# Kernel optimization log

Hardware: AMD Instinct MI355X
Metric: run time of the kernel (lower is better)

## Reference

```python
import jax, jax.numpy as jnp
import numpy as np

EPS = 1e-5  # nn.LayerNorm default
TOP_K = 2


def setup_inputs() -> dict:
    key = jax.random.key(0)
    ks = jax.random.split(key, 8)
    B, S, D, H, E = 4, 2048, 512, 512, 8
    sd = lambda fan_in: 1.0 / np.sqrt(fan_in)
    x = jax.random.normal(ks[0], (B, S, D), dtype=jnp.float32)
    # gate: Linear(D, E, bias=False)
    Wg = jax.random.uniform(ks[1], (D, E), jnp.float32, -sd(D), sd(D))
    # stacked expert params (ExpertModule): fc1 D->H, fc2 H->D, LayerNorm(D)
    W1 = jax.random.uniform(ks[2], (E, D, H), jnp.float32, -sd(D), sd(D))
    b1 = jax.random.uniform(ks[3], (E, H), jnp.float32, -sd(D), sd(D))
    W2 = jax.random.uniform(ks[4], (E, H, D), jnp.float32, -sd(H), sd(H))
    b2 = jax.random.uniform(ks[5], (E, D), jnp.float32, -sd(H), sd(H))
    gamma = jnp.ones((E, D), jnp.float32)
    beta = jnp.zeros((E, D), jnp.float32)
    return {"x": x, "Wg": Wg, "W1": W1, "b1": b1, "W2": W2, "b2": b2,
            "gamma": gamma, "beta": beta}


def _moe_forward(x, Wg, W1, b1, W2, b2, gamma, beta):
    B, S, D = x.shape
    xf = x.reshape(-1, D)                                   # [T, D]
    # gating: top-k logits then softmax over the k selected logits only
    logits = xf @ Wg                                        # [T, E]
    topv, topi = jax.lax.top_k(logits, TOP_K)               # [T, K]
    gate_w = jax.nn.softmax(topv, axis=-1)                  # [T, K]
    # expert MLP + LayerNorm computed for all experts (dropout inactive in eval)
    h = jax.nn.relu(jnp.einsum('td,edh->teh', xf, W1) + b1[None])   # [T, E, H]
    y = jnp.einsum('teh,ehd->ted', h, W2) + b2[None]                 # [T, E, D]
    mu = jnp.mean(y, axis=-1, keepdims=True)
    var = jnp.mean((y - mu) ** 2, axis=-1, keepdims=True)
    y = (y - mu) / jnp.sqrt(var + EPS) * gamma[None] + beta[None]
    # combine: gather the k selected expert outputs and weight-sum
    y_sel = jnp.take_along_axis(y, topi[:, :, None], axis=1)        # [T, K, D]
    out = jnp.sum(gate_w[:, :, None] * y_sel, axis=1)               # [T, D]
    return out.reshape(B, S, D)


def reference(x, Wg, W1, b1, W2, b2, gamma, beta):
    return _moe_forward(x, Wg, W1, b1, W2, b2, gamma, beta)
```

## Files before the change

### kernel.cpp

```cpp
#include <hip/hip_runtime.h>
#include <hip/hip_bf16.h>


#define T_TOK   8192
#define DDIM    512
#define HDIM    512
#define NEXP    8
#define NASSIGN (T_TOK * 2)
#define CPAD    16

typedef _Float16 f16x8 __attribute__((ext_vector_type(8)));
typedef _Float16 f16x4 __attribute__((ext_vector_type(4)));
typedef float    f32x4 __attribute__((ext_vector_type(4)));

__device__ __forceinline__ void gld_lds16(const _Float16* g, _Float16* l) {
    __builtin_amdgcn_global_load_lds(
        (const __attribute__((address_space(1))) unsigned int*)g,
        (__attribute__((address_space(3))) unsigned int*)l,
        16, 0, 0);
}

__global__ __launch_bounds__(256) void prep_kernel(
    const float* __restrict__ x,
    const float* __restrict__ Wg,
    const float* __restrict__ W1,
    const float* __restrict__ W2,
    _Float16* __restrict__ xh,
    int* __restrict__ ei,
    float* __restrict__ gw,
    int* __restrict__ counts,
    _Float16* __restrict__ W1t,
    _Float16* __restrict__ W2t)
{
    __shared__ float wgt[NEXP][512];
    __shared__ float tile[32][33];
    __shared__ int lcnt[NEXP];

    int bid = blockIdx.x;
    int tid = threadIdx.x;

    if (bid < 2048) {
        if (tid < NEXP) lcnt[tid] = 0;
#pragma unroll
        for (int r = 0; r < 2; r++) {
            int d = r * 256 + tid;
            const float4* wr = (const float4*)(Wg + (size_t)d * NEXP);
            float4 a = wr[0], b = wr[1];
            wgt[0][d] = a.x; wgt[1][d] = a.y; wgt[2][d] = a.z; wgt[3][d] = a.w;
            wgt[4][d] = b.x; wgt[5][d] = b.y; wgt[6][d] = b.z; wgt[7][d] = b.w;
        }
        __syncthreads();

        int lane = tid & 63;
        int wave = tid >> 6;
        int t = bid * 4 + wave;

        double acc[NEXP];
#pragma unroll
        for (int e = 0; e < NEXP; e++) acc[e] = 0.0;

#pragma unroll
        for (int jj = 0; jj < 2; jj++) {
            int d0 = jj * 256 + lane * 4;
            float4 xv = *(const float4*)(x + (size_t)t * DDIM + d0);
            f16x4 hv;
            hv[0] = (_Float16)xv.x; hv[1] = (_Float16)xv.y;
            hv[2] = (_Float16)xv.z; hv[3] = (_Float16)xv.w;
            *(f16x4*)(xh + (size_t)t * DDIM + d0) = hv;
            double xd[4] = {(double)xv.x, (double)xv.y, (double)xv.z, (double)xv.w};
#pragma unroll
            for (int e = 0; e < NEXP; e++) {
                f32x4 wv = *(const f32x4*)(&wgt[e][d0]);
#pragma unroll
                for (int c = 0; c < 4; c++)
                    acc[e] += xd[c] * (double)wv[c];
            }
        }
#pragma unroll
        for (int off = 1; off < 8; off <<= 1) {
#pragma unroll
            for (int e = 0; e < NEXP; e++) acc[e] += __shfl_xor(acc[e], off, 64);
        }
        double v = acc[0];
#pragma unroll
        for (int e = 1; e < NEXP; e++) if ((lane & 7) == e) v = acc[e];
#pragma unroll
        for (int off = 8; off < 64; off <<= 1) v += __shfl_xor(v, off, 64);
        double lv[NEXP];
#pragma unroll
        for (int e = 0; e < NEXP; e++) lv[e] = __shfl(v, e, 64);

        double v0 = -1e300; int i0 = 0;
#pragma unroll
        for (int e = 0; e < NEXP; e++) if (lv[e] > v0) { v0 = lv[e]; i0 = e; }
        double v1 = -1e300; int i1 = (i0 == 0) ? 1 : 0;
#pragma unroll
        for (int e = 0; e < NEXP; e++) if (e != i0 && lv[e] > v1) { v1 = lv[e]; i1 = e; }
        if (lane == 0) {
            double ex = exp(v1 - v0);
            float g0 = (float)(1.0 / (1.0 + ex));
            float g1 = (float)(ex / (1.0 + ex));
            ei[2 * t] = i0;  ei[2 * t + 1] = i1;
            gw[2 * t] = g0;  gw[2 * t + 1] = g1;
            atomicAdd(&lcnt[i0], 1);
            atomicAdd(&lcnt[i1], 1);
        }
        __syncthreads();
        if (tid < NEXP) {
            int c = lcnt[tid];
            if (c) atomicAdd(&counts[tid * CPAD], c);
        }
    } else {
        int b2 = bid - 2048;
        int z = b2 >> 8;
        int rem = b2 & 255;
        int by = (rem >> 4) * 32;
        int bx = (rem & 15) * 32;
        const float* src;
        _Float16* dst;
        if (z < 8) { src = W1 + (size_t)z * 512 * 512; dst = W1t + (size_t)z * 512 * 512; }
        else       { src = W2 + (size_t)(z - 8) * 512 * 512; dst = W2t + (size_t)(z - 8) * 512 * 512; }
        int tx = tid & 31, ty = tid >> 5;
#pragma unroll
        for (int i = 0; i < 4; i++) {
            int r = by + ty + i * 8;
            tile[ty + i * 8][tx] = src[(size_t)r * 512 + bx + tx];
        }
        __syncthreads();
        int row = tid >> 3;
        int jc  = tid & 7;
        f16x4 v;
#pragma unroll
        for (int k = 0; k < 4; k++) v[k] = (_Float16)tile[jc * 4 + k][row];
        *(f16x4*)(dst + (size_t)(bx + row) * 512 + by + jc * 4) = v;
    }
}

__global__ void scatter_kernel(const int* __restrict__ ei,
                               const int* __restrict__ counts,
                               int* __restrict__ cursor,
                               int* __restrict__ rowtok,
                               int* __restrict__ pos) {
    int offs[NEXP];
    {
        int s = 0;
#pragma unroll
        for (int q = 0; q < NEXP; q++) { offs[q] = s; s += counts[q * CPAD]; }
    }
    int t = blockIdx.x * 256 + threadIdx.x;
    int lane = threadIdx.x & 63;
#pragma unroll
    for (int k = 0; k < 2; k++) {
        int s = 2 * t + k;
        int e = ei[s];
        int r = 0;
#pragma unroll
        for (int ex = 0; ex < NEXP; ex++) {
            unsigned long long mask = __ballot(e == ex);
            if (e == ex) {
                int leader = __ffsll((unsigned long long)mask) - 1;
                int cnt = __popcll(mask);
                unsigned long long below = mask & ((lane == 63) ? 0x7fffffffffffffffull
                                                                : ((1ull << lane) - 1ull));
                int base = 0;
                if (lane == leader) base = atomicAdd(&cursor[ex * CPAD], cnt);
                base = __shfl(base, leader, 64);
                r = offs[ex] + base + __popcll(below);
            }
        }
        rowtok[r] = s;
        pos[s] = r;
    }
}

template <bool GATHER, bool RELU>
__global__ __launch_bounds__(256) void gemm_tile(
    const _Float16* __restrict__ A,
    const _Float16* __restrict__ Bt,
    const float* __restrict__ bias,
    const int* __restrict__ rowtok,
    const int* __restrict__ counts,
    _Float16* __restrict__ C)
{
    int bid = blockIdx.x;
    int e = bid & 7;
    int j = bid >> 3;
    int ne, off;
    {
        int s = 0; ne = 0; off = 0;
#pragma unroll
        for (int q = 0; q < NEXP; q++) {
            int c = counts[q * CPAD];
            if (q == e) { off = s; ne = c; }
            s += c;
        }
    }
    int m0 = (j >> 2) * 128;
    if (m0 >= ne) return;
    int n0 = (j & 3) * 128;
    const _Float16* Bte = Bt + (size_t)e * 512 * 512;

    __shared__ _Float16 As[2][128 * 32];
    __shared__ _Float16 Bs[2][128 * 32];

    int tid = threadIdx.x;
    int lane = tid & 63;
    int wave = tid >> 6;
    int wm = (wave >> 1) * 64;
    int wn = (wave & 1) * 64;
    int quad = lane >> 4;
    int l16 = lane & 15;

    int srow = tid >> 2;
    int schunk = tid & 3;
    int ksw = (schunk ^ ((srow >> 1) & 3)) * 8;

    int r0g = m0 + srow;
    int r1g = m0 + srow + 64;
    int cr0 = off + (r0g < ne ? r0g : ne - 1);
    int cr1 = off + (r1g < ne ? r1g : ne - 1);
    const _Float16* arow0;
    const _Float16* arow1;
    if (GATHER) {
        arow0 = A + (size_t)(rowtok[cr0] >> 1) * 512;
        arow1 = A + (size_t)(rowtok[cr1] >> 1) * 512;
    } else {
        arow0 = A + (size_t)cr0 * 512;
        arow1 = A + (size_t)cr1 * 512;
    }
    const _Float16* brow0 = Bte + (size_t)(n0 + srow) * 512;
    const _Float16* brow1 = Bte + (size_t)(n0 + srow + 64) * 512;

    f32x4 acc[4][4];
#pragma unroll
    for (int i = 0; i < 4; i++)
#pragma unroll
        for (int jj = 0; jj < 4; jj++) {
            acc[i][jj][0] = 0.f; acc[i][jj][1] = 0.f;
            acc[i][jj][2] = 0.f; acc[i][jj][3] = 0.f;
        }

    int rsw = (quad ^ ((l16 >> 1) & 3)) * 8;

    gld_lds16(arow0 + ksw, &As[0][tid * 8]);
    gld_lds16(arow1 + ksw, &As[0][tid * 8 + 64 * 32]);
    gld_lds16(brow0 + ksw, &Bs[0][tid * 8]);
    gld_lds16(brow1 + ksw, &Bs[0][tid * 8 + 64 * 32]);
    __syncthreads();

    int cur = 0;
    for (int t = 0; t < 16; ++t) {
        if (t < 15) {
            int k1 = (t + 1) * 32;
            gld_lds16(arow0 + k1 + ksw, &As[cur ^ 1][tid * 8]);
            gld_lds16(arow1 + k1 + ksw, &As[cur ^ 1][tid * 8 + 64 * 32]);
            gld_lds16(brow0 + k1 + ksw, &Bs[cur ^ 1][tid * 8]);
            gld_lds16(brow1 + k1 + ksw, &Bs[cur ^ 1][tid * 8 + 64 * 32]);
        }

        f16x8 af[4], bf[4];
#pragma unroll
        for (int i = 0; i < 4; i++)
            af[i] = *(const f16x8*)(&As[cur][(wm + i * 16 + l16) * 32 + rsw]);
#pragma unroll
        for (int jj = 0; jj < 4; jj++)
            bf[jj] = *(const f16x8*)(&Bs[cur][(wn + jj * 16 + l16) * 32 + rsw]);
#pragma unroll
        for (int i = 0; i < 4; i++)
#pragma unroll
            for (int jj = 0; jj < 4; jj++)
                acc[i][jj] = __builtin_amdgcn_mfma_f32_16x16x32_f16(af[i], bf[jj], acc[i][jj], 0, 0, 0);

        if (t < 15) {
            __syncthreads();
            cur ^= 1;
        }
    }

    float bcol[4];
#pragma unroll
    for (int jj = 0; jj < 4; jj++) bcol[jj] = bias[(size_t)e * 512 + n0 + wn + jj * 16 + l16];
#pragma unroll
    for (int i = 0; i < 4; i++) {
#pragma unroll
        for (int rr = 0; rr < 4; rr++) {
            int rg = m0 + wm + i * 16 + quad * 4 + rr;
            if (rg < ne) {
#pragma unroll
                for (int jj = 0; jj < 4; jj++) {
                    float v = acc[i][jj][rr] + bcol[jj];
                    if (RELU) v = fmaxf(v, 0.0f);
                    C[(size_t)(off + rg) * 512 + n0 + wn + jj * 16 + l16] = (_Float16)v;
                }
            }
        }
    }
}

__global__ void ln_combine_kernel(const _Float16* __restrict__ yb,
                                  const int* __restrict__ pos,
                                  const float* __restrict__ gw,
                                  const int* __restrict__ ei,
                                  const float* __restrict__ gamma,
                                  const float* __restrict__ beta,
                                  float* __restrict__ out) {
    int t = blockIdx.x * 4 + (threadIdx.x >> 6);
    int lane = threadIdx.x & 63;
    float o[8];
#pragma unroll
    for (int j = 0; j < 8; j++) o[j] = 0.0f;

#pragma unroll
    for (int k = 0; k < 2; k++) {
        int s = 2 * t + k;
        int r = pos[s];
        int e = ei[s];
        float w = gw[s];
        f16x8 v = *(const f16x8*)(yb + (size_t)r * 512 + lane * 8);
        float f[8];
        float sum = 0.f, sq = 0.f;
#pragma unroll
        for (int j = 0; j < 8; j++) { f[j] = (float)v[j]; sum += f[j]; sq += f[j] * f[j]; }
#pragma unroll
        for (int off = 1; off < 64; off <<= 1) {
            sum += __shfl_xor(sum, off, 64);
            sq  += __shfl_xor(sq, off, 64);
        }
        float mu = sum * (1.0f / 512.0f);
        float var = sq * (1.0f / 512.0f) - mu * mu;
        float rstd = rsqrtf(var + 1e-5f);
#pragma unroll
        for (int j = 0; j < 8; j++) {
            int d = lane * 8 + j;
            o[j] += w * ((f[j] - mu) * rstd * gamma[(size_t)e * 512 + d] + beta[(size_t)e * 512 + d]);
        }
    }
    float4* op = (float4*)(out + (size_t)t * 512 + lane * 8);
    op[0] = make_float4(o[0], o[1], o[2], o[3]);
    op[1] = make_float4(o[4], o[5], o[6], o[7]);
}

extern "C" void kernel_launch(void* const* d_in, const int* in_sizes, int n_in,
                              void* d_out, int out_size, void* d_ws, size_t ws_size,
                              hipStream_t stream) {
    const float* x     = (const float*)d_in[0];
    const float* Wg    = (const float*)d_in[1];
    const float* W1    = (const float*)d_in[2];
    const float* b1    = (const float*)d_in[3];
    const float* W2    = (const float*)d_in[4];
    const float* b2    = (const float*)d_in[5];
    const float* gamma = (const float*)d_in[6];
    const float* beta  = (const float*)d_in[7];
    float* out = (float*)d_out;

    char* w = (char*)d_ws;
    size_t o = 0;
    auto alloc = [&](size_t bytes) -> void* {
        void* p = w + o;
        o += (bytes + 255) & ~(size_t)255;
        return p;
    };
    _Float16* xh  = (_Float16*)alloc((size_t)T_TOK * DDIM * 2);
    _Float16* W1t = (_Float16*)alloc((size_t)NEXP * DDIM * HDIM * 2);
    _Float16* W2t = (_Float16*)alloc((size_t)NEXP * DDIM * HDIM * 2);
    _Float16* hb  = (_Float16*)alloc((size_t)NASSIGN * HDIM * 2);
    _Float16* yb  = (_Float16*)alloc((size_t)NASSIGN * DDIM * 2);
    float* gw     = (float*)alloc((size_t)NASSIGN * 4);
    int* ei       = (int*)alloc((size_t)NASSIGN * 4);
    int* rowtok   = (int*)alloc((size_t)NASSIGN * 4);
    int* pos      = (int*)alloc((size_t)NASSIGN * 4);
    int* counts   = (int*)alloc(NEXP * CPAD * 4);
    int* cursor   = (int*)alloc(NEXP * CPAD * 4);
    (void)ws_size; (void)n_in; (void)in_sizes; (void)out_size;

    hipMemsetAsync(counts, 0, 2 * NEXP * CPAD * sizeof(int), stream);

    prep_kernel<<<6144, 256, 0, stream>>>(x, Wg, W1, W2, xh, ei, gw, counts, W1t, W2t);
    scatter_kernel<<<32, 256, 0, stream>>>(ei, counts, cursor, rowtok, pos);

    gemm_tile<true, true><<<640, 256, 0, stream>>>(xh, W1t, b1, rowtok, counts, hb);
    gemm_tile<false, false><<<640, 256, 0, stream>>>(hb, W2t, b2, nullptr, counts, yb);

    ln_combine_kernel<<<2048, 256, 0, stream>>>(yb, pos, gw, ei, gamma, beta, out);
}
```

Measured before the change: 177.0 us.

## Fuse both expert GEMMs and LayerNorm into one kernel with hidden in LDS

Result: slower. 194.0 us (+9.6%).

```diff
diff --git a/kernel.cpp b/kernel.cpp
--- a/kernel.cpp
+++ b/kernel.cpp
@@ -12,6 +12,13 @@
 typedef _Float16 f16x8 __attribute__((ext_vector_type(8)));
 typedef _Float16 f16x4 __attribute__((ext_vector_type(4)));
 typedef float    f32x4 __attribute__((ext_vector_type(4)));
+
+#define SM_WT   0
+#define SM_XT   65536
+#define SM_H    73728
+#define SM_PS   139264
+#define SM_FS   143360
+#define SM_SIZE 143872
 
 __device__ __forceinline__ void gld_lds16(const _Float16* g, _Float16* l) {
     __builtin_amdgcn_global_load_lds(
@@ -173,18 +180,28 @@
     }
 }
 
-template <bool GATHER, bool RELU>
-__global__ __launch_bounds__(256) void gemm_tile(
-    const _Float16* __restrict__ A,
-    const _Float16* __restrict__ Bt,
-    const float* __restrict__ bias,
+__global__ __launch_bounds__(512, 2) void fused_expert(
+    const _Float16* __restrict__ xh,
+    const _Float16* __restrict__ W1t,
+    const _Float16* __restrict__ W2t,
+    const float* __restrict__ b1,
+    const float* __restrict__ b2,
+    const float* __restrict__ gamma,
+    const float* __restrict__ beta,
     const int* __restrict__ rowtok,
     const int* __restrict__ counts,
-    _Float16* __restrict__ C)
+    _Float16* __restrict__ yb)
 {
+    extern __shared__ char smem[];
+    _Float16* Wt = (_Float16*)(smem + SM_WT);
+    _Float16* Xt = (_Float16*)(smem + SM_XT);
+    char*     Hb = smem + SM_H;
+    float2*   ps = (float2*)(smem + SM_PS);
+    float2*   fs = (float2*)(smem + SM_FS);
+
     int bid = blockIdx.x;
     int e = bid & 7;
-    int j = bid >> 3;
+    int mblk = bid >> 3;
     int ne, off;
     {
         int s = 0; ne = 0; off = 0;
@@ -195,146 +212,227 @@
             s += c;
         }
     }
-    int m0 = (j >> 2) * 128;
+    int m0 = mblk * 64;
     if (m0 >= ne) return;
-    int n0 = (j & 3) * 128;
-    const _Float16* Bte = Bt + (size_t)e * 512 * 512;
-
-    __shared__ _Float16 As[2][128 * 32];
-    __shared__ _Float16 Bs[2][128 * 32];
+
+    const _Float16* W1e = W1t + (size_t)e * 512 * 512;
+    const _Float16* W2e = W2t + (size_t)e * 512 * 512;
 
     int tid = threadIdx.x;
     int lane = tid & 63;
     int wave = tid >> 6;
-    int wm = (wave >> 1) * 64;
-    int wn = (wave & 1) * 64;
     int quad = lane >> 4;
     int l16 = lane & 15;
-
-    int srow = tid >> 2;
-    int schunk = tid & 3;
-    int ksw = (schunk ^ ((srow >> 1) & 3)) * 8;
-
-    int r0g = m0 + srow;
-    int r1g = m0 + srow + 64;
-    int cr0 = off + (r0g < ne ? r0g : ne - 1);
-    int cr1 = off + (r1g < ne ? r1g : ne - 1);
-    const _Float16* arow0;
-    const _Float16* arow1;
-    if (GATHER) {
-        arow0 = A + (size_t)(rowtok[cr0] >> 1) * 512;
-        arow1 = A + (size_t)(rowtok[cr1] >> 1) * 512;
-    } else {
-        arow0 = A + (size_t)cr0 * 512;
-        arow1 = A + (size_t)cr1 * 512;
-    }
-    const _Float16* brow0 = Bte + (size_t)(n0 + srow) * 512;
-    const _Float16* brow1 = Bte + (size_t)(n0 + srow + 64) * 512;
-
-    f32x4 acc[4][4];
+    int wm = wave * 64;
+
+    int swrow = tid >> 2;
+    int kswW = ((tid & 3) ^ ((swrow >> 1) & 3)) * 8;
+
+    const _Float16* axrow = xh;
+    int kswX = 0;
+    if (tid < 256) {
+        int xr = tid >> 2;
+        int rg = m0 + xr;
+        int cr = off + (rg < ne ? rg : ne - 1);
+        axrow = xh + (size_t)(rowtok[cr] >> 1) * 512;
+        kswX = ((tid & 3) ^ ((xr >> 1) & 3)) * 8;
+    }
+
+    int rsw = (quad ^ ((l16 >> 1) & 3)) * 8;
+
+    auto STAGE_W = [&](int buf, const _Float16* Wb, int k0) {
+#pragma unroll
+        for (int it = 0; it < 4; it++)
+            gld_lds16(Wb + (size_t)(it * 128 + swrow) * 512 + k0 + kswW,
+                      Wt + buf * 16384 + it * 128 * 32 + tid * 8);
+    };
+    auto STAGE_X = [&](int buf, int k0) {
+        if (tid < 256)
+            gld_lds16(axrow + k0 + kswX, Xt + buf * 2048 + tid * 8);
+    };
+
+    f32x4 acc1[4][4];
 #pragma unroll
     for (int i = 0; i < 4; i++)
 #pragma unroll
-        for (int jj = 0; jj < 4; jj++) {
-            acc[i][jj][0] = 0.f; acc[i][jj][1] = 0.f;
-            acc[i][jj][2] = 0.f; acc[i][jj][3] = 0.f;
-        }
-
-    int rsw = (quad ^ ((l16 >> 1) & 3)) * 8;
-
-    gld_lds16(arow0 + ksw, &As[0][tid * 8]);
-    gld_lds16(arow1 + ksw, &As[0][tid * 8 + 64 * 32]);
-    gld_lds16(brow0 + ksw, &Bs[0][tid * 8]);
-    gld_lds16(brow1 + ksw, &Bs[0][tid * 8 + 64 * 32]);
-    __syncthreads();
-
+        for (int j = 0; j < 4; j++) {
+            acc1[i][j][0] = 0.f; acc1[i][j][1] = 0.f;
+            acc1[i][j][2] = 0.f; acc1[i][j][3] = 0.f;
+        }
+
+    STAGE_W(0, W1e, 0);
+    STAGE_X(0, 0);
+    __syncthreads();
     int cur = 0;
     for (int t = 0; t < 16; ++t) {
-        if (t < 15) {
-            int k1 = (t + 1) * 32;
-            gld_lds16(arow0 + k1 + ksw, &As[cur ^ 1][tid * 8]);
-            gld_lds16(arow1 + k1 + ksw, &As[cur ^ 1][tid * 8 + 64 * 32]);
-            gld_lds16(brow0 + k1 + ksw, &Bs[cur ^ 1][tid * 8]);
-            gld_lds16(brow1 + k1 + ksw, &Bs[cur ^ 1][tid * 8 + 64 * 32]);
-        }
-
+        if (t < 15) { STAGE_W(cur ^ 1, W1e, (t + 1) * 32); STAGE_X(cur ^ 1, (t + 1) * 32); }
         f16x8 af[4], bf[4];
 #pragma unroll
         for (int i = 0; i < 4; i++)
-            af[i] = *(const f16x8*)(&As[cur][(wm + i * 16 + l16) * 32 + rsw]);
-#pragma unroll
-        for (int jj = 0; jj < 4; jj++)
-            bf[jj] = *(const f16x8*)(&Bs[cur][(wn + jj * 16 + l16) * 32 + rsw]);
+            af[i] = *(const f16x8*)(&Wt[cur * 16384 + (wm + i * 16 + l16) * 32 + rsw]);
+#pragma unroll
+        for (int j = 0; j < 4; j++)
+            bf[j] = *(const f16x8*)(&Xt[cur * 2048 + (j * 16 + l16) * 32 + rsw]);
 #pragma unroll
         for (int i = 0; i < 4; i++)
 #pragma unroll
-            for (int jj = 0; jj < 4; jj++)
-                acc[i][jj] = __builtin_amdgcn_mfma_f32_16x16x32_f16(af[i], bf[jj], acc[i][jj], 0, 0, 0);
-
-        if (t < 15) {
-            __syncthreads();
-            cur ^= 1;
-        }
-    }
-
-    float bcol[4];
-#pragma unroll
-    for (int jj = 0; jj < 4; jj++) bcol[jj] = bias[(size_t)e * 512 + n0 + wn + jj * 16 + l16];
+            for (int j = 0; j < 4; j++)
+                acc1[i][j] = __builtin_amdgcn_mfma_f32_16x16x32_f16(af[i], bf[j], acc1[i][j], 0, 0, 0);
+        if (t < 15) { __syncthreads(); cur ^= 1; }
+    }
+
+    {
+        float b1v[16];
+#pragma unroll
+        for (int i = 0; i < 4; i++)
+#pragma unroll
+            for (int rr = 0; rr < 4; rr++)
+                b1v[i * 4 + rr] = b1[(size_t)e * 512 + wm + i * 16 + quad * 4 + rr];
+#pragma unroll
+        for (int i = 0; i < 4; i++) {
+#pragma unroll
+            for (int j = 0; j < 4; j++) {
+                int r = j * 16 + l16;
+                int ch = ((wm >> 3) + i * 2 + (quad >> 1)) ^ (r & 7);
+                f16x4 hv;
+#pragma unroll
+                for (int rr = 0; rr < 4; rr++)
+                    hv[rr] = (_Float16)fmaxf(acc1[i][j][rr] + b1v[i * 4 + rr], 0.0f);
+                *(f16x4*)(Hb + r * 1024 + ch * 16 + (quad & 1) * 8) = hv;
+            }
+        }
+    }
+    __syncthreads();
+
+    f32x4 acc2[4][4];
+#pragma unroll
+    for (int i = 0; i < 4; i++)
+#pragma unroll
+        for (int j = 0; j < 4; j++) {
+            acc2[i][j][0] = 0.f; acc2[i][j][1] = 0.f;
+            acc2[i][j][2] = 0.f; acc2[i][j][3] = 0.f;
+        }
+
+    STAGE_W(0, W2e, 0);
+    __syncthreads();
+    cur = 0;
+    for (int t = 0; t < 16; ++t) {
+        if (t < 15) STAGE_W(cur ^ 1, W2e, (t + 1) * 32);
+        f16x8 af2[4], bf2[4];
+#pragma unroll
+        for (int i = 0; i < 4; i++) {
+            int r = i * 16 + l16;
+            int ch = ((t * 4) + quad) ^ (r & 7);
+            af2[i] = *(const f16x8*)(Hb + r * 1024 + ch * 16);
+        }
+#pragma unroll
+        for (int j = 0; j < 4; j++)
+            bf2[j] = *(const f16x8*)(&Wt[cur * 16384 + (wm + j * 16 + l16) * 32 + rsw]);
+#pragma unroll
+        for (int i = 0; i < 4; i++)
+#pragma unroll
+            for (int j = 0; j < 4; j++)
+                acc2[i][j] = __builtin_amdgcn_mfma_f32_16x16x32_f16(af2[i], bf2[j], acc2[i][j], 0, 0, 0);
+        if (t < 15) { __syncthreads(); cur ^= 1; }
+    }
+
+    float b2v[4], gv[4], bv[4];
+#pragma unroll
+    for (int j = 0; j < 4; j++) {
+        int d = wm + j * 16 + l16;
+        b2v[j] = b2[(size_t)e * 512 + d];
+        gv[j]  = gamma[(size_t)e * 512 + d];
+        bv[j]  = beta[(size_t)e * 512 + d];
+    }
+    float sum_[16], sq_[16];
+#pragma unroll
+    for (int i = 0; i < 4; i++)
+#pragma unroll
+        for (int rr = 0; rr < 4; rr++) {
+            float s = 0.f, q2 = 0.f;
+#pragma unroll
+            for (int j = 0; j < 4; j++) {
+                float v = acc2[i][j][rr] + b2v[j];
+                s += v; q2 += v * v;
+            }
+            sum_[i * 4 + rr] = s; sq_[i * 4 + rr] = q2;
+        }
+#pragma unroll
+    for (int off2 = 1; off2 < 16; off2 <<= 1) {
+#pragma unroll
+        for (int k = 0; k < 16; k++) {
+            sum_[k] += __shfl_xor(sum_[k], off2, 64);
+            sq_[k]  += __shfl_xor(sq_[k],  off2, 64);
+        }
+    }
+    __syncthreads();
+    if (l16 == 0) {
+#pragma unroll
+        for (int i = 0; i < 4; i++)
+#pragma unroll
+            for (int rr = 0; rr < 4; rr++) {
+                int r = i * 16 + quad * 4 + rr;
+                ps[wave * 64 + r] = make_float2(sum_[i * 4 + rr], sq_[i * 4 + rr]);
+            }
+    }
+    __syncthreads();
+    if (tid < 64) {
+        float a = 0.f, b = 0.f;
+#pragma unroll
+        for (int w2 = 0; w2 < 8; w2++) {
+            float2 p = ps[w2 * 64 + tid];
+            a += p.x; b += p.y;
+        }
+        fs[tid] = make_float2(a, b);
+    }
+    __syncthreads();
+
 #pragma unroll
     for (int i = 0; i < 4; i++) {
 #pragma unroll
         for (int rr = 0; rr < 4; rr++) {
-            int rg = m0 + wm + i * 16 + quad * 4 + rr;
-            if (rg < ne) {
-#pragma unroll
-                for (int jj = 0; jj < 4; jj++) {
-                    float v = acc[i][jj][rr] + bcol[jj];
-                    if (RELU) v = fmaxf(v, 0.0f);
-                    C[(size_t)(off + rg) * 512 + n0 + wn + jj * 16 + l16] = (_Float16)v;
-                }
-            }
-        }
-    }
-}
-
-__global__ void ln_combine_kernel(const _Float16* __restrict__ yb,
-                                  const int* __restrict__ pos,
-                                  const float* __restrict__ gw,
-                                  const int* __restrict__ ei,
-                                  const float* __restrict__ gamma,
-                                  const float* __restrict__ beta,
-                                  float* __restrict__ out) {
+            int r = i * 16 + quad * 4 + rr;
+            float2 st = fs[r];
+            float mu = st.x * (1.0f / 512.0f);
+            float var = st.y * (1.0f / 512.0f) - mu * mu;
+            float rstd = rsqrtf(var + 1e-5f);
+#pragma unroll
+            for (int j = 0; j < 4; j++) {
+                int d = wm + j * 16 + l16;
+                float v = (acc2[i][j][rr] + b2v[j] - mu) * rstd * gv[j] + bv[j];
+                *(_Float16*)(Hb + r * 1024 + ((d * 2) ^ (quad << 5))) = (_Float16)v;
+            }
+        }
+    }
+    __syncthreads();
+
+#pragma unroll
+    for (int s = 0; s < 8; s++) {
+        int idx = s * 512 + tid;
+        int r = idx >> 6;
+        int wq = (r >> 2) & 3;
+        int wb = (idx & 63) * 16;
+        if (m0 + r < ne) {
+            f16x8 v = *(const f16x8*)(Hb + r * 1024 + (wb ^ (wq << 5)));
+            *(f16x8*)(yb + (size_t)(off + m0 + r) * 512 + (wb >> 1)) = v;
+        }
+    }
+}
+
+__global__ void combine_kernel(const _Float16* __restrict__ yb,
+                               const int* __restrict__ pos,
+                               const float* __restrict__ gw,
+                               float* __restrict__ out) {
     int t = blockIdx.x * 4 + (threadIdx.x >> 6);
     int lane = threadIdx.x & 63;
+    int s0 = 2 * t, s1 = 2 * t + 1;
+    int r0 = pos[s0], r1 = pos[s1];
+    float g0 = gw[s0], g1 = gw[s1];
+    f16x8 a = *(const f16x8*)(yb + (size_t)r0 * 512 + lane * 8);
+    f16x8 b = *(const f16x8*)(yb + (size_t)r1 * 512 + lane * 8);
     float o[8];
 #pragma unroll
-    for (int j = 0; j < 8; j++) o[j] = 0.0f;
-
-#pragma unroll
-    for (int k = 0; k < 2; k++) {
-        int s = 2 * t + k;
-        int r = pos[s];
-        int e = ei[s];
-        float w = gw[s];
-        f16x8 v = *(const f16x8*)(yb + (size_t)r * 512 + lane * 8);
-        float f[8];
-        float sum = 0.f, sq = 0.f;
-#pragma unroll
-        for (int j = 0; j < 8; j++) { f[j] = (float)v[j]; sum += f[j]; sq += f[j] * f[j]; }
-#pragma unroll
-        for (int off = 1; off < 64; off <<= 1) {
-            sum += __shfl_xor(sum, off, 64);
-            sq  += __shfl_xor(sq, off, 64);
-        }
-        float mu = sum * (1.0f / 512.0f);
-        float var = sq * (1.0f / 512.0f) - mu * mu;
-        float rstd = rsqrtf(var + 1e-5f);
-#pragma unroll
-        for (int j = 0; j < 8; j++) {
-            int d = lane * 8 + j;
-            o[j] += w * ((f[j] - mu) * rstd * gamma[(size_t)e * 512 + d] + beta[(size_t)e * 512 + d]);
-        }
-    }
+    for (int j = 0; j < 8; j++) o[j] = g0 * (float)a[j] + g1 * (float)b[j];
     float4* op = (float4*)(out + (size_t)t * 512 + lane * 8);
     op[0] = make_float4(o[0], o[1], o[2], o[3]);
     op[1] = make_float4(o[4], o[5], o[6], o[7]);
@@ -363,7 +461,6 @@
     _Float16* xh  = (_Float16*)alloc((size_t)T_TOK * DDIM * 2);
     _Float16* W1t = (_Float16*)alloc((size_t)NEXP * DDIM * HDIM * 2);
     _Float16* W2t = (_Float16*)alloc((size_t)NEXP * DDIM * HDIM * 2);
-    _Float16* hb  = (_Float16*)alloc((size_t)NASSIGN * HDIM * 2);
     _Float16* yb  = (_Float16*)alloc((size_t)NASSIGN * DDIM * 2);
     float* gw     = (float*)alloc((size_t)NASSIGN * 4);
     int* ei       = (int*)alloc((size_t)NASSIGN * 4);
@@ -373,13 +470,20 @@
     int* cursor   = (int*)alloc(NEXP * CPAD * 4);
     (void)ws_size; (void)n_in; (void)in_sizes; (void)out_size;
 
+    static bool s_attr = false;
+    if (!s_attr) {
+        hipFuncSetAttribute((const void*)fused_expert,
+                            hipFuncAttributeMaxDynamicSharedMemorySize, SM_SIZE);
+        s_attr = true;
+    }
+
     hipMemsetAsync(counts, 0, 2 * NEXP * CPAD * sizeof(int), stream);
 
     prep_kernel<<<6144, 256, 0, stream>>>(x, Wg, W1, W2, xh, ei, gw, counts, W1t, W2t);
     scatter_kernel<<<32, 256, 0, stream>>>(ei, counts, cursor, rowtok, pos);
 
-    gemm_tile<true, true><<<640, 256, 0, stream>>>(xh, W1t, b1, rowtok, counts, hb);
-    gemm_tile<false, false><<<640, 256, 0, stream>>>(hb, W2t, b2, nullptr, counts, yb);
-
-    ln_combine_kernel<<<2048, 256, 0, stream>>>(yb, pos, gw, ei, gamma, beta, out);
-}
+    fused_expert<<<1024, 512, SM_SIZE, stream>>>(xh, W1t, W2t, b1, b2, gamma, beta,
+                                                 rowtok, counts, yb);
+
+    combine_kernel<<<2048, 256, 0, stream>>>(yb, pos, gw, out);
+}
```

## Fuse token scatter into gating kernel and use 64-row GEMM tiles

Applied to the files above, without the earlier changes.

After: 167.5 us. 5.4% less time.

```diff
diff --git a/kernel.cpp b/kernel.cpp
--- a/kernel.cpp
+++ b/kernel.cpp
@@ -8,6 +8,8 @@
 #define NEXP    8
 #define NASSIGN (T_TOK * 2)
 #define CPAD    16
+#define CAP     4096
+#define MT      40
 
 typedef _Float16 f16x8 __attribute__((ext_vector_type(8)));
 typedef _Float16 f16x4 __attribute__((ext_vector_type(4)));
@@ -28,13 +30,16 @@
     _Float16* __restrict__ xh,
     int* __restrict__ ei,
     float* __restrict__ gw,
-    int* __restrict__ counts,
+    int* __restrict__ cursor,
+    int* __restrict__ rowtok,
+    int* __restrict__ pos,
     _Float16* __restrict__ W1t,
     _Float16* __restrict__ W2t)
 {
     __shared__ float wgt[NEXP][512];
     __shared__ float tile[32][33];
     __shared__ int lcnt[NEXP];
+    __shared__ int gbase[NEXP];
 
     int bid = blockIdx.x;
     int tid = threadIdx.x;
@@ -96,19 +101,28 @@
         double v1 = -1e300; int i1 = (i0 == 0) ? 1 : 0;
 #pragma unroll
         for (int e = 0; e < NEXP; e++) if (e != i0 && lv[e] > v1) { v1 = lv[e]; i1 = e; }
+
+        int lr0 = 0, lr1 = 0;
         if (lane == 0) {
             double ex = exp(v1 - v0);
             float g0 = (float)(1.0 / (1.0 + ex));
             float g1 = (float)(ex / (1.0 + ex));
             ei[2 * t] = i0;  ei[2 * t + 1] = i1;
             gw[2 * t] = g0;  gw[2 * t + 1] = g1;
-            atomicAdd(&lcnt[i0], 1);
-            atomicAdd(&lcnt[i1], 1);
+            lr0 = atomicAdd(&lcnt[i0], 1);
+            lr1 = atomicAdd(&lcnt[i1], 1);
         }
         __syncthreads();
         if (tid < NEXP) {
             int c = lcnt[tid];
-            if (c) atomicAdd(&counts[tid * CPAD], c);
+            gbase[tid] = c ? atomicAdd(&cursor[tid * CPAD], c) : 0;
+        }
+        __syncthreads();
+        if (lane == 0) {
+            int r0 = i0 * CAP + gbase[i0] + lr0;
+            int r1 = i1 * CAP + gbase[i1] + lr1;
+            rowtok[r0] = 2 * t;      pos[2 * t] = r0;
+            rowtok[r1] = 2 * t + 1;  pos[2 * t + 1] = r1;
         }
     } else {
         int b2 = bid - 2048;
@@ -136,104 +150,50 @@
     }
 }
 
-__global__ void scatter_kernel(const int* __restrict__ ei,
-                               const int* __restrict__ counts,
-                               int* __restrict__ cursor,
-                               int* __restrict__ rowtok,
-                               int* __restrict__ pos) {
-    int offs[NEXP];
-    {
-        int s = 0;
-#pragma unroll
-        for (int q = 0; q < NEXP; q++) { offs[q] = s; s += counts[q * CPAD]; }
-    }
-    int t = blockIdx.x * 256 + threadIdx.x;
-    int lane = threadIdx.x & 63;
-#pragma unroll
-    for (int k = 0; k < 2; k++) {
-        int s = 2 * t + k;
-        int e = ei[s];
-        int r = 0;
-#pragma unroll
-        for (int ex = 0; ex < NEXP; ex++) {
-            unsigned long long mask = __ballot(e == ex);
-            if (e == ex) {
-                int leader = __ffsll((unsigned long long)mask) - 1;
-                int cnt = __popcll(mask);
-                unsigned long long below = mask & ((lane == 63) ? 0x7fffffffffffffffull
-                                                                : ((1ull << lane) - 1ull));
-                int base = 0;
-                if (lane == leader) base = atomicAdd(&cursor[ex * CPAD], cnt);
-                base = __shfl(base, leader, 64);
-                r = offs[ex] + base + __popcll(below);
-            }
-        }
-        rowtok[r] = s;
-        pos[s] = r;
-    }
-}
-
 template <bool GATHER, bool RELU>
 __global__ __launch_bounds__(256) void gemm_tile(
     const _Float16* __restrict__ A,
     const _Float16* __restrict__ Bt,
     const float* __restrict__ bias,
     const int* __restrict__ rowtok,
-    const int* __restrict__ counts,
+    const int* __restrict__ cursor,
     _Float16* __restrict__ C)
 {
     int bid = blockIdx.x;
     int e = bid & 7;
     int j = bid >> 3;
-    int ne, off;
-    {
-        int s = 0; ne = 0; off = 0;
-#pragma unroll
-        for (int q = 0; q < NEXP; q++) {
-            int c = counts[q * CPAD];
-            if (q == e) { off = s; ne = c; }
-            s += c;
-        }
-    }
-    int m0 = (j >> 2) * 128;
+    int ne = cursor[e * CPAD];
+    int m0 = (j >> 2) * 64;
     if (m0 >= ne) return;
     int n0 = (j & 3) * 128;
+    int off = e * CAP;
     const _Float16* Bte = Bt + (size_t)e * 512 * 512;
 
-    __shared__ _Float16 As[2][128 * 32];
+    __shared__ _Float16 As[2][64 * 32];
     __shared__ _Float16 Bs[2][128 * 32];
 
     int tid = threadIdx.x;
     int lane = tid & 63;
     int wave = tid >> 6;
-    int wm = (wave >> 1) * 64;
+    int wm = (wave >> 1) * 32;
     int wn = (wave & 1) * 64;
     int quad = lane >> 4;
     int l16 = lane & 15;
 
     int srow = tid >> 2;
-    int schunk = tid & 3;
-    int ksw = (schunk ^ ((srow >> 1) & 3)) * 8;
-
-    int r0g = m0 + srow;
-    int r1g = m0 + srow + 64;
-    int cr0 = off + (r0g < ne ? r0g : ne - 1);
-    int cr1 = off + (r1g < ne ? r1g : ne - 1);
-    const _Float16* arow0;
-    const _Float16* arow1;
-    if (GATHER) {
-        arow0 = A + (size_t)(rowtok[cr0] >> 1) * 512;
-        arow1 = A + (size_t)(rowtok[cr1] >> 1) * 512;
-    } else {
-        arow0 = A + (size_t)cr0 * 512;
-        arow1 = A + (size_t)cr1 * 512;
-    }
+    int ksw = ((tid & 3) ^ ((srow >> 1) & 3)) * 8;
+
+    int rg0 = m0 + srow;
+    int cr0 = off + (rg0 < ne ? rg0 : ne - 1);
+    const _Float16* arow;
+    if (GATHER) arow = A + (size_t)(rowtok[cr0] >> 1) * 512;
+    else        arow = A + (size_t)cr0 * 512;
     const _Float16* brow0 = Bte + (size_t)(n0 + srow) * 512;
     const _Float16* brow1 = Bte + (size_t)(n0 + srow + 64) * 512;
 
-    f32x4 acc[4][4];
-#pragma unroll
-    for (int i = 0; i < 4; i++)
+    f32x4 acc[2][4];
+#pragma unroll
+    for (int i = 0; i < 2; i++)
 #pragma unroll
         for (int jj = 0; jj < 4; jj++) {
             acc[i][jj][0] = 0.f; acc[i][jj][1] = 0.f;
@@ -242,8 +202,7 @@
 
     int rsw = (quad ^ ((l16 >> 1) & 3)) * 8;
 
-    gld_lds16(arow0 + ksw, &As[0][tid * 8]);
-    gld_lds16(arow1 + ksw, &As[0][tid * 8 + 64 * 32]);
+    gld_lds16(arow + ksw, &As[0][tid * 8]);
     gld_lds16(brow0 + ksw, &Bs[0][tid * 8]);
     gld_lds16(brow1 + ksw, &Bs[0][tid * 8 + 64 * 32]);
     __syncthreads();
@@ -252,21 +211,20 @@
     for (int t = 0; t < 16; ++t) {
         if (t < 15) {
             int k1 = (t + 1) * 32;
-            gld_lds16(arow0 + k1 + ksw, &As[cur ^ 1][tid * 8]);
-            gld_lds16(arow1 + k1 + ksw, &As[cur ^ 1][tid * 8 + 64 * 32]);
+            gld_lds16(arow + k1 + ksw, &As[cur ^ 1][tid * 8]);
             gld_lds16(brow0 + k1 + ksw, &Bs[cur ^ 1][tid * 8]);
             gld_lds16(brow1 + k1 + ksw, &Bs[cur ^ 1][tid * 8 + 64 * 32]);
         }
 
-        f16x8 af[4], bf[4];
-#pragma unroll
-        for (int i = 0; i < 4; i++)
+        f16x8 af[2], bf[4];
+#pragma unroll
+        for (int i = 0; i < 2; i++)
             af[i] = *(const f16x8*)(&As[cur][(wm + i * 16 + l16) * 32 + rsw]);
 #pragma unroll
         for (int jj = 0; jj < 4; jj++)
             bf[jj] = *(const f16x8*)(&Bs[cur][(wn + jj * 16 + l16) * 32 + rsw]);
 #pragma unroll
-        for (int i = 0; i < 4; i++)
+        for (int i = 0; i < 2; i++)
 #pragma unroll
             for (int jj = 0; jj < 4; jj++)
                 acc[i][jj] = __builtin_amdgcn_mfma_f32_16x16x32_f16(af[i], bf[jj], acc[i][jj], 0, 0, 0);
@@ -281,7 +239,7 @@
 #pragma unroll
     for (int jj = 0; jj < 4; jj++) bcol[jj] = bias[(size_t)e * 512 + n0 + wn + jj * 16 + l16];
 #pragma unroll
-    for (int i = 0; i < 4; i++) {
+    for (int i = 0; i < 2; i++) {
 #pragma unroll
         for (int rr = 0; rr < 4; rr++) {
             int rg = m0 + wm + i * 16 + quad * 4 + rr;
@@ -363,23 +321,22 @@
     _Float16* xh  = (_Float16*)alloc((size_t)T_TOK * DDIM * 2);
     _Float16* W1t = (_Float16*)alloc((size_t)NEXP * DDIM * HDIM * 2);
     _Float16* W2t = (_Float16*)alloc((size_t)NEXP * DDIM * HDIM * 2);
-    _Float16* hb  = (_Float16*)alloc((size_t)NASSIGN * HDIM * 2);
-    _Float16* yb  = (_Float16*)alloc((size_t)NASSIGN * DDIM * 2);
+    _Float16* hb  = (_Float16*)alloc((size_t)NEXP * CAP * HDIM * 2);
+    _Float16* yb  = (_Float16*)alloc((size_t)NEXP * CAP * DDIM * 2);
     float* gw     = (float*)alloc((size_t)NASSIGN * 4);
     int* ei       = (int*)alloc((size_t)NASSIGN * 4);
-    int* rowtok   = (int*)alloc((size_t)NASSIGN * 4);
+    int* rowtok   = (int*)alloc((size_t)NEXP * CAP * 4);
     int* pos      = (int*)alloc((size_t)NASSIGN * 4);
-    int* counts   = (int*)alloc(NEXP * CPAD * 4);
     int* cursor   = (int*)alloc(NEXP * CPAD * 4);
     (void)ws_size; (void)n_in; (void)in_sizes; (void)out_size;
 
-    hipMemsetAsync(counts, 0, 2 * NEXP * CPAD * sizeof(int), stream);
-
-    prep_kernel<<<6144, 256, 0, stream>>>(x, Wg, W1, W2, xh, ei, gw, counts, W1t, W2t);
-    scatter_kernel<<<32, 256, 0, stream>>>(ei, counts, cursor, rowtok, pos);
-
-    gemm_tile<true, true><<<640, 256, 0, stream>>>(xh, W1t, b1, rowtok, counts, hb);
-    gemm_tile<false, false><<<640, 256, 0, stream>>>(hb, W2t, b2, nullptr, counts, yb);
+    hipMemsetAsync(cursor, 0, NEXP * CPAD * sizeof(int), stream);
+
+    prep_kernel<<<6144, 256, 0, stream>>>(x, Wg, W1, W2, xh, ei, gw,
+                                          cursor, rowtok, pos, W1t, W2t);
+
+    gemm_tile<true, true><<<1280, 256, 0, stream>>>(xh, W1t, b1, rowtok, cursor, hb);
+    gemm_tile<false, false><<<1280, 256, 0, stream>>>(hb, W2t, b2, nullptr, cursor, yb);
 
     ln_combine_kernel<<<2048, 256, 0, stream>>>(yb, pos, gw, ei, gamma, beta, out);
 }
```
